# Performance work log

Hardware: AMD Instinct MI355X
Metric: run time of the kernel (lower is better)

Reference implementation:

```python
import jax, jax.numpy as jnp
import numpy as np

DV = 512   # node feature size
DE = 256   # edge feature size
N = 128    # valid node num (human_nums + obj_nums)
B = 8
K = 3      # propagate_layers
C = 117    # hoi_classes


def gru_cell(x, h, w_ih, w_hh, b_ih, b_hh):
    # PyTorch nn.GRU single step, gate order (r, z, n)
    gi = w_ih @ x + b_ih
    gh = w_hh @ h + b_hh
    ir, iz, inn = jnp.split(gi, 3)
    hr, hz, hn = jnp.split(gh, 3)
    r = jax.nn.sigmoid(ir + hr)
    z = jax.nn.sigmoid(iz + hz)
    n = jnp.tanh(inn + r * hn)
    return (1.0 - z) * n + z * h


def _run_graph(h, e, w_link, b_link, w_msg, b_msg, w_ih, w_hh, b_ih, b_hh):
    # h: [dv, N], e: [de, N, N]
    wl_j = w_link[:DV]          # applied to Feature[:dv, i, :] = h (column index j)
    wl_i = w_link[DV:2 * DV]    # applied to Feature[dv:2dv, :, i] = h (row index i)
    wl_e = w_link[2 * DV:]
    adj = jnp.zeros((N, N), h.dtype)
    for _ in range(K):
        # link function on Feature built under torch.no_grad -> stop_gradient
        hs = jax.lax.stop_gradient(h)
        es = jax.lax.stop_gradient(e)
        logits = (wl_i @ hs)[:, None] + (wl_j @ hs)[None, :] \
                 + jnp.einsum('c,cij->ij', wl_e, es) + b_link
        adj = jax.nn.sigmoid(logits)  # [N, N]

        def node_step(carry, i):
            h, e = carry
            h_v = h[:, i]                      # [dv]
            e_row = e[:, i, :]                 # [de, N] (rows < i already updated this round)
            comb = jnp.concatenate(
                [jnp.broadcast_to(h_v[:, None], (DV, N)), h, e_row], axis=0)  # [2dv+de, N]
            m = jax.nn.relu(w_msg @ comb + b_msg[:, None])                    # [de, N]
            e = e.at[:, i, :].set(m)
            m_sum = (m * adj[i][None, :]).sum(axis=1)                         # [de]
            h_new = gru_cell(m_sum, h_v, w_ih, w_hh, b_ih, b_hh)
            h = h.at[:, i].set(h_new)
            return (h, e), None

        (h, e), _ = jax.lax.scan(node_step, (h, e), jnp.arange(N))
    return adj, h


def setup_inputs() -> dict:
    key = jax.random.key(0)
    ks = jax.random.split(key, 8)
    s = 0.02
    return {
        "edge_features": jax.random.normal(ks[0], (B, N, N, DE), jnp.float32),
        "node_features": jax.random.normal(ks[1], (B, N, DV), jnp.float32),
        "adj_mat": jnp.zeros((B, N, N), jnp.float32),
        "node_labels": jnp.zeros((B, N, C), jnp.float32),
        "human_nums": jnp.full((B,), 32, jnp.int32),
        "obj_nums": jnp.full((B,), 96, jnp.int32),
        "w_link": jax.random.normal(ks[2], (2 * DV + DE,), jnp.float32) * s,
        "b_link": jnp.zeros((), jnp.float32),
        "w_msg": jax.random.normal(ks[3], (DE, 2 * DV + DE), jnp.float32) * s,
        "b_msg": jnp.zeros((DE,), jnp.float32),
        "w_ih": jax.random.normal(ks[4], (3 * DV, DE), jnp.float32) * s,
        "w_hh": jax.random.normal(ks[5], (3 * DV, DV), jnp.float32) * s,
        "b_ih": jnp.zeros((3 * DV,), jnp.float32),
        "b_hh": jnp.zeros((3 * DV,), jnp.float32),
        "w_ro": jax.random.normal(ks[6], (C, DV), jnp.float32) * s,
        "b_ro": jnp.zeros((C,), jnp.float32),
    }


def reference(edge_features, node_features, adj_mat, node_labels, human_nums,
              obj_nums, w_link, b_link, w_msg, b_msg, w_ih, w_hh, b_ih, b_hh,
              w_ro, b_ro):
    e0 = jnp.transpose(edge_features, (0, 3, 1, 2))  # [B, de, N, N]
    h0 = jnp.transpose(node_features, (0, 2, 1))     # [B, dv, N]
    run = jax.vmap(_run_graph, in_axes=(0, 0) + (None,) * 8)
    pred_adj_mat, h = run(h0, e0, w_link, b_link, w_msg, b_msg,
                          w_ih, w_hh, b_ih, b_hh)
    # readout on the final (post-last-update) node states
    pred_node_labels = jnp.einsum('cd,bdn->bnc', w_ro, h) + b_ro
    return pred_adj_mat, pred_node_labels
```

## Files before the change

kernel.cpp:

```cpp
#include <hip/hip_runtime.h>
#include <math.h>


#define NB 8
#define NN 128
#define DVV 512
#define DEE 256
#define NCC 117
#define SB 16
#define PGOFF 196608

typedef __attribute__((ext_vector_type(8))) short short8;
typedef __attribute__((ext_vector_type(4))) float f32x4;

__device__ __forceinline__ float sigmf(float x) {
  x = fminf(fmaxf(x, -30.f), 30.f);
  return 1.0f / (1.0f + __expf(-x));
}
__device__ __forceinline__ float tanhf_fast(float x) {
  x = fminf(fmaxf(x, -15.f), 15.f);
  float e = __expf(2.0f * x);
  return (e - 1.0f) / (e + 1.0f);
}
__device__ __forceinline__ unsigned short f2bf(float f) {
  union { float f; unsigned u; } v; v.f = f;
  unsigned u = v.u + 0x7FFFu + ((v.u >> 16) & 1u);
  return (unsigned short)(u >> 16);
}

__global__ __launch_bounds__(256) void k_copy(const float* __restrict__ src, float* __restrict__ dst) {
  int i = blockIdx.x * 256 + threadIdx.x;
  ((float4*)dst)[i] = ((const float4*)src)[i];
}

__global__ __launch_bounds__(256) void k_cvtw(const float* __restrict__ w_msg,
                                              unsigned short* __restrict__ w3b) {
  int idx = blockIdx.x * 256 + threadIdx.x;
  int r = idx >> 8, c = idx & 255;
  w3b[idx] = f2bf(w_msg[(size_t)r * 1280 + 1024 + c]);
}

__global__ __launch_bounds__(128) void k_av(const float* __restrict__ h, const float* __restrict__ w_link,
                                            float* __restrict__ av) {
  int b = blockIdx.x >> 7, n = blockIdx.x & 127;
  int lane = threadIdx.x & 63, half = threadIdx.x >> 6;
  const float* hc = h + (size_t)((b << 7) + n) * DVV;
  const float* w = w_link + half * DVV;
  float acc = 0.f;
#pragma unroll
  for (int t = 0; t < 8; ++t) { int d = lane + (t << 6); acc += w[d] * hc[d]; }
#pragma unroll
  for (int off = 32; off; off >>= 1) acc += __shfl_down(acc, off);
  if (lane == 0) av[(b << 8) + half * NN + n] = acc;
}

template <int FIRST>
__global__ __launch_bounds__(256) void k_plogit_mfma(
    const float* src, const unsigned short* __restrict__ w3b,
    const float* __restrict__ w_link, const float* __restrict__ av,
    const float* __restrict__ b_link, float* e_buf, float* __restrict__ adj_out) {
  int b = blockIdx.x >> 7, i = blockIdx.x & 127;
  __shared__ unsigned short eL[128 * 264];
  int tid = threadIdx.x;

  if (FIRST) {
    const float* s0 = src + (size_t)(b * NN + i) * NN * DEE;
    int j = tid >> 6, c0 = (tid & 63) * 4;
#pragma unroll 4
    for (int it = 0; it < 32; ++it, j += 4) {
      float4 v = *(const float4*)&s0[(size_t)j * DEE + c0];
      unsigned long long pk = (unsigned long long)f2bf(v.x)
                            | ((unsigned long long)f2bf(v.y) << 16)
                            | ((unsigned long long)f2bf(v.z) << 32)
                            | ((unsigned long long)f2bf(v.w) << 48);
      *(unsigned long long*)&eL[j * 264 + c0] = pk;
    }
  } else {
    const float* s0 = src + (size_t)(b * NN + i) * DEE * NN;
    int j0 = (tid & 31) * 4, c0b = (tid >> 5) * 4;
#pragma unroll
    for (int it = 0; it < 8; ++it) {
      int c0 = c0b + 32 * it;
      float4 r0 = *(const float4*)&s0[(size_t)(c0 + 0) * NN + j0];
      float4 r1 = *(const float4*)&s0[(size_t)(c0 + 1) * NN + j0];
      float4 r2 = *(const float4*)&s0[(size_t)(c0 + 2) * NN + j0];
      float4 r3 = *(const float4*)&s0[(size_t)(c0 + 3) * NN + j0];
      unsigned long long p0 = (unsigned long long)f2bf(r0.x) | ((unsigned long long)f2bf(r1.x) << 16)
                            | ((unsigned long long)f2bf(r2.x) << 32) | ((unsigned long long)f2bf(r3.x) << 48);
      unsigned long long p1 = (unsigned long long)f2bf(r0.y) | ((unsigned long long)f2bf(r1.y) << 16)
                            | ((unsigned long long)f2bf(r2.y) << 32) | ((unsigned long long)f2bf(r3.y) << 48);
      unsigned long long p2 = (unsigned long long)f2bf(r0.z) | ((unsigned long long)f2bf(r1.z) << 16)
                            | ((unsigned long long)f2bf(r2.z) << 32) | ((unsigned long long)f2bf(r3.z) << 48);
      unsigned long long p3 = (unsigned long long)f2bf(r0.w) | ((unsigned long long)f2bf(r1.w) << 16)
                            | ((unsigned long long)f2bf(r2.w) << 32) | ((unsigned long long)f2bf(r3.w) << 48);
      *(unsigned long long*)&eL[(j0 + 0) * 264 + c0] = p0;
      *(unsigned long long*)&eL[(j0 + 1) * 264 + c0] = p1;
      *(unsigned long long*)&eL[(j0 + 2) * 264 + c0] = p2;
      *(unsigned long long*)&eL[(j0 + 3) * 264 + c0] = p3;
    }
  }
  __syncthreads();

  float accLE = 0.f;
  if (tid < NN) {
    const unsigned short* row = &eL[tid * 264];
    for (int c = 0; c < DEE; ++c) {
      union { unsigned u; float f; } cv; cv.u = ((unsigned)row[c]) << 16;
      accLE += w_link[1024 + c] * cv.f;
    }
  }

  const int w = tid >> 6, l = tid & 63;
  const int lm = l & 15, lg = l >> 4;
  f32x4 acc[4][8];
#pragma unroll
  for (int a = 0; a < 4; ++a)
#pragma unroll
    for (int jt = 0; jt < 8; ++jt) acc[a][jt] = (f32x4){0.f, 0.f, 0.f, 0.f};

#pragma unroll
  for (int kk = 0; kk < 8; ++kk) {
    short8 afr[4];
#pragma unroll
    for (int a = 0; a < 4; ++a)
      afr[a] = *(const short8*)&w3b[(size_t)(64 * w + 16 * a + lm) * 256 + 32 * kk + 8 * lg];
#pragma unroll
    for (int jt = 0; jt < 8; ++jt) {
      short8 bfr = *(const short8*)&eL[(16 * jt + lm) * 264 + 32 * kk + 8 * lg];
#pragma unroll
      for (int a = 0; a < 4; ++a)
        acc[a][jt] = __builtin_amdgcn_mfma_f32_16x16x32_bf16(afr[a], bfr, acc[a][jt], 0, 0, 0);
    }
  }

  float* Pout = e_buf + (size_t)(b * NN + i) * DEE * NN;
#pragma unroll
  for (int a = 0; a < 4; ++a) {
    int rbase = 64 * w + 16 * a + 4 * lg;
#pragma unroll
    for (int jt = 0; jt < 8; ++jt) {
      int j = 16 * jt + lm;
#pragma unroll
      for (int q = 0; q < 4; ++q)
        Pout[(size_t)(rbase + q) * NN + j] = acc[a][jt][q];
    }
  }
  if (tid < NN) {
    float x = av[(b << 8) + NN + i] + av[(b << 8) + tid] + accLE + b_link[0];
    adj_out[((size_t)b * NN + i) * NN + tid] = sigmf(x);
  }
}

__global__ __launch_bounds__(256) void k_wh3(const float* __restrict__ w_hh, const float* __restrict__ w_msg,
                                             const float* __restrict__ b_hh, const float* __restrict__ b_msg,
                                             const float* __restrict__ h, float* __restrict__ GHo,
                                             float* __restrict__ Uo, float* __restrict__ Go) {
  int bx = blockIdx.x, b = blockIdx.y;
  const float* W; const float* bias; float* out; int ldw, R, r0;
  if (bx < 96)       { W = w_hh;        ldw = 512;  R = 1536; bias = b_hh;   out = GHo; r0 = bx * 16; }
  else if (bx < 112) { W = w_msg;       ldw = 1280; R = 256;  bias = b_msg;  out = Uo;  r0 = (bx - 96) * 16; }
  else               { W = w_msg + 512; ldw = 1280; R = 256;  bias = nullptr; out = Go; r0 = (bx - 112) * 16; }
  __shared__ float hT[128][129];
  __shared__ float wT[16][129];
  __shared__ float outT[16][129];
  int tid = threadIdx.x;
  int n = tid & 127, rr = tid >> 7;
  float acc8[8] = {0, 0, 0, 0, 0, 0, 0, 0};
  for (int dc = 0; dc < DVV; dc += 128) {
    if (dc) __syncthreads();
    for (int l = tid * 4; l < 16384; l += 1024) {
      int nn = l >> 7, d = l & 127;
      float4 v = *(const float4*)&h[((size_t)(b << 7) + nn) * DVV + dc + d];
      hT[d + 0][nn] = v.x; hT[d + 1][nn] = v.y; hT[d + 2][nn] = v.z; hT[d + 3][nn] = v.w;
    }
    for (int l = tid; l < 2048; l += 256) {
      int r = l >> 7, d = l & 127;
      wT[r][d] = W[(size_t)(r0 + r) * ldw + dc + d];
    }
    __syncthreads();
    for (int d = 0; d < 128; ++d) {
      float hval = hT[d][n];
#pragma unroll
      for (int r8 = 0; r8 < 8; ++r8) acc8[r8] += wT[rr * 8 + r8][d] * hval;
    }
  }
#pragma unroll
  for (int r8 = 0; r8 < 8; ++r8) {
    int r = rr * 8 + r8;
    outT[r][n] = acc8[r8] + (bias ? bias[r0 + r] : 0.0f);
  }
  __syncthreads();
  int n2 = tid >> 1, q = tid & 1;
  size_t base = ((size_t)(b << 7) + n2) * R + r0 + q * 8;
  float4 o0; o0.x = outT[q * 8 + 0][n2]; o0.y = outT[q * 8 + 1][n2]; o0.z = outT[q * 8 + 2][n2]; o0.w = outT[q * 8 + 3][n2];
  float4 o1; o1.x = outT[q * 8 + 4][n2]; o1.y = outT[q * 8 + 5][n2]; o1.z = outT[q * 8 + 6][n2]; o1.w = outT[q * 8 + 7][n2];
  *(float4*)&out[base] = o0;
  *(float4*)&out[base + 4] = o1;
}

template <int WRITE_E>
__global__ __launch_bounds__(256) void k_scan8(
    float* eP, const float* __restrict__ adj, const float* __restrict__ GH,
    const float* __restrict__ U, const float* __restrict__ Gini, float* __restrict__ h,
    const float* __restrict__ w_ih, const float* __restrict__ b_ih,
    const float* __restrict__ w_msg, float* __restrict__ pg,
    unsigned* __restrict__ flags, int kround) {
  const int s = blockIdx.x, b = blockIdx.y, tid = threadIdx.x;
  __shared__ float wihL[16 * 1540];
  __shared__ __align__(16) float w2L[16 * 520];
  __shared__ __align__(16) float GL[16 * 132];
  __shared__ float hnL[DVV];
  __shared__ float msL[16];

  for (int l = tid; l < 1536 * 16; l += 256) {
    int r = l >> 4, c = l & 15;
    wihL[c * 1540 + r] = w_ih[(size_t)r * 256 + 16 * s + c];
  }
  for (int l = tid; l < 16 * 128; l += 256) {
    int c = l >> 7, d4 = (l & 127) * 4;
    *(float4*)&w2L[c * 520 + d4] = *(const float4*)&w_msg[(size_t)(16 * s + c) * 1280 + 512 + d4];
  }
  for (int l = tid; l < 2048; l += 256) {
    int c = l & 15, j = l >> 4;
    GL[c * 132 + j] = Gini[((size_t)b * NN + j) * DEE + 16 * s + c];
  }
  float bi0 = b_ih[tid], bi1 = b_ih[tid + 256];
  float bi2 = b_ih[512 + tid], bi3 = b_ih[768 + tid];
  float bi4 = b_ih[1024 + tid], bi5 = b_ih[1280 + tid];

  const int c_loc = tid >> 4, jg = tid & 15, j0 = jg << 3;

  float4 P0, P1, A0, A1; float uu;
  float hv0, hv1, ghr0, ghr1, ghz0, ghz1, ghn0, ghn1;
  {
    size_t rE = ((size_t)(b * NN + 0) * DEE + 16 * s + c_loc) * NN + j0;
    P0 = *(const float4*)&eP[rE]; P1 = *(const float4*)&eP[rE + 4];
    size_t rA = (size_t)(b * NN + 0) * NN + j0;
    A0 = *(const float4*)&adj[rA]; A1 = *(const float4*)&adj[rA + 4];
    uu = U[(size_t)(b * NN + 0) * DEE + 16 * s + c_loc];
    size_t rH = (size_t)(b * NN + 0) * DVV;
    hv0 = h[rH + tid]; hv1 = h[rH + tid + 256];
    size_t rG = (size_t)(b * NN + 0) * 1536;
    ghr0 = GH[rG + tid]; ghr1 = GH[rG + tid + 256];
    ghz0 = GH[rG + 512 + tid]; ghz1 = GH[rG + 768 + tid];
    ghn0 = GH[rG + 1024 + tid]; ghn1 = GH[rG + 1280 + tid];
  }

  for (int i = 0; i < NN; ++i) {
    float* pgb = pg + (size_t)(i & 1) * PGOFF + (size_t)((b << 4) + s) * 1536;
    float* pgr = pg + (size_t)(i & 1) * PGOFF + (size_t)(b << 4) * 1536;
    __syncthreads();

    float acc;
    {
      const float* gl = &GL[c_loc * 132 + j0];
      float4 g0 = *(const float4*)&gl[0];
      float4 g1 = *(const float4*)&gl[4];
      float m0 = fmaxf(uu + g0.x + P0.x, 0.f), m1 = fmaxf(uu + g0.y + P0.y, 0.f);
      float m2 = fmaxf(uu + g0.z + P0.z, 0.f), m3 = fmaxf(uu + g0.w + P0.w, 0.f);
      float m4 = fmaxf(uu + g1.x + P1.x, 0.f), m5 = fmaxf(uu + g1.y + P1.y, 0.f);
      float m6 = fmaxf(uu + g1.z + P1.z, 0.f), m7 = fmaxf(uu + g1.w + P1.w, 0.f);
      acc = A0.x * m0 + A0.y * m1 + A0.z * m2 + A0.w * m3
          + A1.x * m4 + A1.y * m5 + A1.z * m6 + A1.w * m7;
      if (WRITE_E) {
        size_t rE = ((size_t)(b * NN + i) * DEE + 16 * s + c_loc) * NN + j0;
        float4 w0; w0.x = m0; w0.y = m1; w0.z = m2; w0.w = m3;
        float4 w1; w1.x = m4; w1.y = m5; w1.z = m6; w1.w = m7;
        *(float4*)&eP[rE] = w0; *(float4*)&eP[rE + 4] = w1;
      }
    }
    {
      int in = (i < NN - 1) ? i + 1 : NN - 1;
      size_t rE = ((size_t)(b * NN + in) * DEE + 16 * s + c_loc) * NN + j0;
      P0 = *(const float4*)&eP[rE]; P1 = *(const float4*)&eP[rE + 4];
      size_t rA = (size_t)(b * NN + in) * NN + j0;
      A0 = *(const float4*)&adj[rA]; A1 = *(const float4*)&adj[rA + 4];
      uu = U[(size_t)(b * NN + in) * DEE + 16 * s + c_loc];
    }
    acc += __shfl_down(acc, 8);
    acc += __shfl_down(acc, 4);
    acc += __shfl_down(acc, 2);
    acc += __shfl_down(acc, 1);
    if (jg == 0) msL[c_loc] = acc;
    __syncthreads();

    {
      float ms[16];
#pragma unroll
      for (int c = 0; c < 16; ++c) ms[c] = msL[c];
#pragma unroll
      for (int u = 0; u < 6; ++u) {
        int r = tid + (u << 8);
        float pa = 0.f;
#pragma unroll
        for (int c = 0; c < 16; ++c) pa += wihL[c * 1540 + r] * ms[c];
        __hip_atomic_store(&pgb[r], pa, __ATOMIC_RELAXED, __HIP_MEMORY_SCOPE_SYSTEM);
      }
    }

    {
      unsigned tgt = (unsigned)(kround * NN + i + 1);
      __syncthreads();
      if (tid < 64) {
        if (tid == 0)
          __hip_atomic_store(&flags[(((b << 4) + s) << 5)], tgt, __ATOMIC_RELAXED,
                             __HIP_MEMORY_SCOPE_SYSTEM);
        unsigned* fp = &flags[(((b << 4) + (tid & 15)) << 5)];
        for (;;) {
          unsigned v = __hip_atomic_load(fp, __ATOMIC_RELAXED, __HIP_MEMORY_SCOPE_SYSTEM);
          if (!__any(v < tgt)) break;
          __builtin_amdgcn_s_sleep(1);
        }
      }
      __syncthreads();
    }

    {
      float sr0 = bi0, sr1 = bi1, sz0 = bi2, sz1 = bi3, sn0 = bi4, sn1 = bi5;
#pragma unroll
      for (int ss = 0; ss < 16; ++ss) {
        float* p = pgr + (size_t)ss * 1536;
        sr0 += __hip_atomic_load(&p[tid],        __ATOMIC_RELAXED, __HIP_MEMORY_SCOPE_SYSTEM);
        sr1 += __hip_atomic_load(&p[tid + 256],  __ATOMIC_RELAXED, __HIP_MEMORY_SCOPE_SYSTEM);
        sz0 += __hip_atomic_load(&p[512 + tid],  __ATOMIC_RELAXED, __HIP_MEMORY_SCOPE_SYSTEM);
        sz1 += __hip_atomic_load(&p[768 + tid],  __ATOMIC_RELAXED, __HIP_MEMORY_SCOPE_SYSTEM);
        sn0 += __hip_atomic_load(&p[1024 + tid], __ATOMIC_RELAXED, __HIP_MEMORY_SCOPE_SYSTEM);
        sn1 += __hip_atomic_load(&p[1280 + tid], __ATOMIC_RELAXED, __HIP_MEMORY_SCOPE_SYSTEM);
      }
      float rg0 = sigmf(sr0 + ghr0), rg1 = sigmf(sr1 + ghr1);
      float z0 = sigmf(sz0 + ghz0),  z1 = sigmf(sz1 + ghz1);
      float nv0 = tanhf_fast(sn0 + rg0 * ghn0);
      float nv1 = tanhf_fast(sn1 + rg1 * ghn1);
      float hn0 = (1.f - z0) * nv0 + z0 * hv0;
      float hn1 = (1.f - z1) * nv1 + z1 * hv1;
      hnL[tid] = hn0; hnL[tid + 256] = hn1;
      size_t rH = (size_t)(b * NN + i) * DVV;
      if ((tid >> 5) == s) h[rH + tid] = hn0;
      if (((tid + 256) >> 5) == s) h[rH + tid + 256] = hn1;
    }
    {
      int in = (i < NN - 1) ? i + 1 : NN - 1;
      size_t rH = (size_t)(b * NN + in) * DVV;
      hv0 = h[rH + tid]; hv1 = h[rH + tid + 256];
      size_t rG = (size_t)(b * NN + in) * 1536;
      ghr0 = GH[rG + tid]; ghr1 = GH[rG + tid + 256];
      ghz0 = GH[rG + 512 + tid]; ghz1 = GH[rG + 768 + tid];
      ghn0 = GH[rG + 1024 + tid]; ghn1 = GH[rG + 1280 + tid];
    }
    __syncthreads();

    {
      int cw = tid >> 4, dg = tid & 15;
      float acc2 = 0.f;
#pragma unroll
      for (int it = 0; it < 32; ++it) {
        int d = dg + (it << 4);
        acc2 += w2L[cw * 520 + d] * hnL[d];
      }
      acc2 += __shfl_down(acc2, 8);
      acc2 += __shfl_down(acc2, 4);
      acc2 += __shfl_down(acc2, 2);
      acc2 += __shfl_down(acc2, 1);
      if (dg == 0) GL[cw * 132 + i] = acc2;
    }
  }
}

__global__ __launch_bounds__(128) void k_labels(const float* __restrict__ h, const float* __restrict__ w_ro,
                                                const float* __restrict__ b_ro, float* __restrict__ out) {
  int b = blockIdx.x >> 7, n = blockIdx.x & 127;
  __shared__ __align__(16) float hr[512];
  int tid = threadIdx.x;
  *(float4*)&hr[tid * 4] = *(const float4*)&h[(size_t)((b << 7) + n) * DVV + tid * 4];
  __syncthreads();
  if (tid < NCC) {
    const float* w = w_ro + (size_t)tid * DVV;
    float acc = b_ro[tid];
    for (int d = 0; d < DVV; d += 4) {
      float4 wv = *(const float4*)&w[d];
      acc += wv.x * hr[d] + wv.y * hr[d + 1] + wv.z * hr[d + 2] + wv.w * hr[d + 3];
    }
    out[(size_t)((b << 7) + n) * NCC + tid] = acc;
  }
}

extern "C" void kernel_launch(void* const* d_in, const int* in_sizes, int n_in,
                              void* d_out, int out_size, void* d_ws, size_t ws_size,
                              hipStream_t stream) {
  const float* edge   = (const float*)d_in[0];
  const float* node   = (const float*)d_in[1];
  const float* w_link = (const float*)d_in[6];
  const float* b_link = (const float*)d_in[7];
  const float* w_msg  = (const float*)d_in[8];
  const float* b_msg  = (const float*)d_in[9];
  const float* w_ih   = (const float*)d_in[10];
  const float* w_hh   = (const float*)d_in[11];
  const float* b_ih   = (const float*)d_in[12];
  const float* b_hh   = (const float*)d_in[13];
  const float* w_ro   = (const float*)d_in[14];
  const float* b_ro   = (const float*)d_in[15];
  float* out = (float*)d_out;
  float* ws  = (float*)d_ws;

  float* e_buf  = ws;
  float* h_buf  = e_buf + 33554432ull;
  float* GH_buf = h_buf + 524288;
  float* U_buf  = GH_buf + 1572864;
  float* G_buf  = U_buf + 262144;
  float* lE_buf = G_buf + 262144;
  float* av_buf = lE_buf + 131072;
  float* pg_buf = av_buf + 2048;
  unsigned* flags = (unsigned*)(pg_buf + 2 * PGOFF);
  unsigned short* w3b = (unsigned short*)lE_buf;
  size_t need_bytes = 36710304ull * 4ull;
  if (ws_size < need_bytes) return;

  hipMemsetAsync(flags, 0, 4096 * sizeof(unsigned), stream);
  k_copy<<<512, 256, 0, stream>>>(node, h_buf);
  k_cvtw<<<256, 256, 0, stream>>>(w_msg, w3b);

  for (int k = 0; k < 3; ++k) {
    k_av<<<1024, 128, 0, stream>>>(h_buf, w_link, av_buf);
    if (k == 0) k_plogit_mfma<1><<<1024, 256, 0, stream>>>(edge, w3b, w_link, av_buf, b_link, e_buf, out);
    else        k_plogit_mfma<0><<<1024, 256, 0, stream>>>(e_buf, w3b, w_link, av_buf, b_link, e_buf, out);
    k_wh3<<<dim3(128, 8), 256, 0, stream>>>(w_hh, w_msg, b_hh, b_msg, h_buf, GH_buf, U_buf, G_buf);
    if (k < 2) k_scan8<1><<<dim3(SB, NB), 256, 0, stream>>>(e_buf, out, GH_buf, U_buf, G_buf, h_buf,
                                                            w_ih, b_ih, w_msg, pg_buf, flags, k);
    else       k_scan8<0><<<dim3(SB, NB), 256, 0, stream>>>(e_buf, out, GH_buf, U_buf, G_buf, h_buf,
                                                            w_ih, b_ih, w_msg, pg_buf, flags, k);
  }
  k_labels<<<1024, 128, 0, stream>>>(h_buf, w_ro, b_ro, out + 131072);
}
```

Before: 2.313 ms.

## Store edge workspace in bf16 to halve edge buffer traffic

The large per-edge projection/message buffer moves from fp32 to bf16 storage. The plogit kernel writes bf16 and reads it back with a short8 transpose into LDS, and the scan kernel loads and stores short8 instead of two float4s. A bf16 copy of h is also kept, though nothing reads it yet. This cuts memory traffic on the dominant edge buffer, at the cost of extra rounding error in the stored messages that compounds across the three rounds.

New measurement: 2.310 ms. About the same (-0.1%).

```diff
diff --git a/kernel.cpp b/kernel.cpp
--- a/kernel.cpp
+++ b/kernel.cpp
@@ -27,10 +27,18 @@
   unsigned u = v.u + 0x7FFFu + ((v.u >> 16) & 1u);
   return (unsigned short)(u >> 16);
 }
-
-__global__ __launch_bounds__(256) void k_copy(const float* __restrict__ src, float* __restrict__ dst) {
+__device__ __forceinline__ float bfu(unsigned short u) {
+  union { unsigned u; float f; } v; v.u = ((unsigned)u) << 16; return v.f;
+}
+
+__global__ __launch_bounds__(256) void k_copy(const float* __restrict__ src, float* __restrict__ dst,
+                                              unsigned short* __restrict__ hb) {
   int i = blockIdx.x * 256 + threadIdx.x;
-  ((float4*)dst)[i] = ((const float4*)src)[i];
+  float4 v = ((const float4*)src)[i];
+  ((float4*)dst)[i] = v;
+  unsigned long long pk = (unsigned long long)f2bf(v.x) | ((unsigned long long)f2bf(v.y) << 16)
+                        | ((unsigned long long)f2bf(v.z) << 32) | ((unsigned long long)f2bf(v.w) << 48);
+  *(unsigned long long*)&hb[i * 4] = pk;
 }
 
 __global__ __launch_bounds__(256) void k_cvtw(const float* __restrict__ w_msg,
@@ -56,47 +64,43 @@
 
 template <int FIRST>
 __global__ __launch_bounds__(256) void k_plogit_mfma(
-    const float* src, const unsigned short* __restrict__ w3b,
+    const float* edge, const unsigned short* eP16in, const unsigned short* __restrict__ w3b,
     const float* __restrict__ w_link, const float* __restrict__ av,
-    const float* __restrict__ b_link, float* e_buf, float* __restrict__ adj_out) {
+    const float* __restrict__ b_link, unsigned short* eP16out, float* __restrict__ adj_out) {
   int b = blockIdx.x >> 7, i = blockIdx.x & 127;
   __shared__ unsigned short eL[128 * 264];
   int tid = threadIdx.x;
 
   if (FIRST) {
-    const float* s0 = src + (size_t)(b * NN + i) * NN * DEE;
-    int j = tid >> 6, c0 = (tid & 63) * 4;
-#pragma unroll 4
-    for (int it = 0; it < 32; ++it, j += 4) {
-      float4 v = *(const float4*)&s0[(size_t)j * DEE + c0];
-      unsigned long long pk = (unsigned long long)f2bf(v.x)
-                            | ((unsigned long long)f2bf(v.y) << 16)
-                            | ((unsigned long long)f2bf(v.z) << 32)
-                            | ((unsigned long long)f2bf(v.w) << 48);
-      *(unsigned long long*)&eL[j * 264 + c0] = pk;
+    const float* s0 = edge + (size_t)(b * NN + i) * NN * DEE;
+    for (int l = tid; l < 4096; l += 256) {
+      int j = l >> 5, c0 = (l & 31) * 8;
+      float4 v0 = *(const float4*)&s0[(size_t)j * DEE + c0];
+      float4 v1 = *(const float4*)&s0[(size_t)j * DEE + c0 + 4];
+      unsigned long long p0 = (unsigned long long)f2bf(v0.x) | ((unsigned long long)f2bf(v0.y) << 16)
+                            | ((unsigned long long)f2bf(v0.z) << 32) | ((unsigned long long)f2bf(v0.w) << 48);
+      unsigned long long p1 = (unsigned long long)f2bf(v1.x) | ((unsigned long long)f2bf(v1.y) << 16)
+                            | ((unsigned long long)f2bf(v1.z) << 32) | ((unsigned long long)f2bf(v1.w) << 48);
+      *(unsigned long long*)&eL[j * 264 + c0] = p0;
+      *(unsigned long long*)&eL[j * 264 + c0 + 4] = p1;
     }
   } else {
-    const float* s0 = src + (size_t)(b * NN + i) * DEE * NN;
-    int j0 = (tid & 31) * 4, c0b = (tid >> 5) * 4;
-#pragma unroll
-    for (int it = 0; it < 8; ++it) {
-      int c0 = c0b + 32 * it;
-      float4 r0 = *(const float4*)&s0[(size_t)(c0 + 0) * NN + j0];
-      float4 r1 = *(const float4*)&s0[(size_t)(c0 + 1) * NN + j0];
-      float4 r2 = *(const float4*)&s0[(size_t)(c0 + 2) * NN + j0];
-      float4 r3 = *(const float4*)&s0[(size_t)(c0 + 3) * NN + j0];
-      unsigned long long p0 = (unsigned long long)f2bf(r0.x) | ((unsigned long long)f2bf(r1.x) << 16)
-                            | ((unsigned long long)f2bf(r2.x) << 32) | ((unsigned long long)f2bf(r3.x) << 48);
-      unsigned long long p1 = (unsigned long long)f2bf(r0.y) | ((unsigned long long)f2bf(r1.y) << 16)
-                            | ((unsigned long long)f2bf(r2.y) << 32) | ((unsigned long long)f2bf(r3.y) << 48);
-      unsigned long long p2 = (unsigned long long)f2bf(r0.z) | ((unsigned long long)f2bf(r1.z) << 16)
-                            | ((unsigned long long)f2bf(r2.z) << 32) | ((unsigned long long)f2bf(r3.z) << 48);
-      unsigned long long p3 = (unsigned long long)f2bf(r0.w) | ((unsigned long long)f2bf(r1.w) << 16)
-                            | ((unsigned long long)f2bf(r2.w) << 32) | ((unsigned long long)f2bf(r3.w) << 48);
-      *(unsigned long long*)&eL[(j0 + 0) * 264 + c0] = p0;
-      *(unsigned long long*)&eL[(j0 + 1) * 264 + c0] = p1;
-      *(unsigned long long*)&eL[(j0 + 2) * 264 + c0] = p2;
-      *(unsigned long long*)&eL[(j0 + 3) * 264 + c0] = p3;
+    const unsigned short* s0 = eP16in + (size_t)(b * NN + i) * DEE * NN;
+#pragma unroll
+    for (int t = 0; t < 2; ++t) {
+      int blk = tid + t * 256;
+      int c0 = (blk >> 4) * 8, j0 = (blk & 15) * 8;
+      short8 rows[8];
+#pragma unroll
+      for (int cc = 0; cc < 8; ++cc)
+        rows[cc] = *(const short8*)&s0[(size_t)(c0 + cc) * NN + j0];
+#pragma unroll
+      for (int jj = 0; jj < 8; ++jj) {
+        short8 o;
+#pragma unroll
+        for (int cc = 0; cc < 8; ++cc) o[cc] = rows[cc][jj];
+        *(short8*)&eL[(j0 + jj) * 264 + c0] = o;
+      }
     }
   }
   __syncthreads();
@@ -104,10 +108,7 @@
   float accLE = 0.f;
   if (tid < NN) {
     const unsigned short* row = &eL[tid * 264];
-    for (int c = 0; c < DEE; ++c) {
-      union { unsigned u; float f; } cv; cv.u = ((unsigned)row[c]) << 16;
-      accLE += w_link[1024 + c] * cv.f;
-    }
+    for (int c = 0; c < DEE; ++c) accLE += w_link[1024 + c] * bfu(row[c]);
   }
 
   const int w = tid >> 6, l = tid & 63;
@@ -133,7 +134,7 @@
     }
   }
 
-  float* Pout = e_buf + (size_t)(b * NN + i) * DEE * NN;
+  unsigned short* Pout = eP16out + (size_t)(b * NN + i) * DEE * NN;
 #pragma unroll
   for (int a = 0; a < 4; ++a) {
     int rbase = 64 * w + 16 * a + 4 * lg;
@@ -142,7 +143,7 @@
       int j = 16 * jt + lm;
 #pragma unroll
       for (int q = 0; q < 4; ++q)
-        Pout[(size_t)(rbase + q) * NN + j] = acc[a][jt][q];
+        Pout[(size_t)(rbase + q) * NN + j] = f2bf(acc[a][jt][q]);
     }
   }
   if (tid < NN) {
@@ -199,12 +200,12 @@
 }
 
 template <int WRITE_E>
-__global__ __launch_bounds__(256) void k_scan8(
-    float* eP, const float* __restrict__ adj, const float* __restrict__ GH,
+__global__ __launch_bounds__(256) void k_scan10(
+    unsigned short* eP16, const float* __restrict__ adj, const float* __restrict__ GH,
     const float* __restrict__ U, const float* __restrict__ Gini, float* __restrict__ h,
-    const float* __restrict__ w_ih, const float* __restrict__ b_ih,
-    const float* __restrict__ w_msg, float* __restrict__ pg,
-    unsigned* __restrict__ flags, int kround) {
+    unsigned short* __restrict__ hb, const float* __restrict__ w_ih,
+    const float* __restrict__ b_ih, const float* __restrict__ w_msg,
+    float* __restrict__ pg, unsigned* __restrict__ flags, int kround) {
   const int s = blockIdx.x, b = blockIdx.y, tid = threadIdx.x;
   __shared__ float wihL[16 * 1540];
   __shared__ __align__(16) float w2L[16 * 520];
@@ -230,11 +231,11 @@
 
   const int c_loc = tid >> 4, jg = tid & 15, j0 = jg << 3;
 
-  float4 P0, P1, A0, A1; float uu;
+  short8 Pv; float4 A0, A1; float uu;
   float hv0, hv1, ghr0, ghr1, ghz0, ghz1, ghn0, ghn1;
   {
     size_t rE = ((size_t)(b * NN + 0) * DEE + 16 * s + c_loc) * NN + j0;
-    P0 = *(const float4*)&eP[rE]; P1 = *(const float4*)&eP[rE + 4];
+    Pv = *(const short8*)&eP16[rE];
     size_t rA = (size_t)(b * NN + 0) * NN + j0;
     A0 = *(const float4*)&adj[rA]; A1 = *(const float4*)&adj[rA + 4];
     uu = U[(size_t)(b * NN + 0) * DEE + 16 * s + c_loc];
@@ -256,23 +257,28 @@
       const float* gl = &GL[c_loc * 132 + j0];
       float4 g0 = *(const float4*)&gl[0];
       float4 g1 = *(const float4*)&gl[4];
-      float m0 = fmaxf(uu + g0.x + P0.x, 0.f), m1 = fmaxf(uu + g0.y + P0.y, 0.f);
-      float m2 = fmaxf(uu + g0.z + P0.z, 0.f), m3 = fmaxf(uu + g0.w + P0.w, 0.f);
-      float m4 = fmaxf(uu + g1.x + P1.x, 0.f), m5 = fmaxf(uu + g1.y + P1.y, 0.f);
-      float m6 = fmaxf(uu + g1.z + P1.z, 0.f), m7 = fmaxf(uu + g1.w + P1.w, 0.f);
+      float m0 = fmaxf(uu + g0.x + bfu((unsigned short)Pv[0]), 0.f);
+      float m1 = fmaxf(uu + g0.y + bfu((unsigned short)Pv[1]), 0.f);
+      float m2 = fmaxf(uu + g0.z + bfu((unsigned short)Pv[2]), 0.f);
+      float m3 = fmaxf(uu + g0.w + bfu((unsigned short)Pv[3]), 0.f);
+      float m4 = fmaxf(uu + g1.x + bfu((unsigned short)Pv[4]), 0.f);
+      float m5 = fmaxf(uu + g1.y + bfu((unsigned short)Pv[5]), 0.f);
+      float m6 = fmaxf(uu + g1.z + bfu((unsigned short)Pv[6]), 0.f);
+      float m7 = fmaxf(uu + g1.w + bfu((unsigned short)Pv[7]), 0.f);
       acc = A0.x * m0 + A0.y * m1 + A0.z * m2 + A0.w * m3
           + A1.x * m4 + A1.y * m5 + A1.z * m6 + A1.w * m7;
       if (WRITE_E) {
         size_t rE = ((size_t)(b * NN + i) * DEE + 16 * s + c_loc) * NN + j0;
-        float4 w0; w0.x = m0; w0.y = m1; w0.z = m2; w0.w = m3;
-        float4 w1; w1.x = m4; w1.y = m5; w1.z = m6; w1.w = m7;
-        *(float4*)&eP[rE] = w0; *(float4*)&eP[rE + 4] = w1;
+        short8 mw;
+        mw[0] = (short)f2bf(m0); mw[1] = (short)f2bf(m1); mw[2] = (short)f2bf(m2); mw[3] = (short)f2bf(m3);
+        mw[4] = (short)f2bf(m4); mw[5] = (short)f2bf(m5); mw[6] = (short)f2bf(m6); mw[7] = (short)f2bf(m7);
+        *(short8*)&eP16[rE] = mw;
       }
     }
     {
       int in = (i < NN - 1) ? i + 1 : NN - 1;
       size_t rE = ((size_t)(b * NN + in) * DEE + 16 * s + c_loc) * NN + j0;
-      P0 = *(const float4*)&eP[rE]; P1 = *(const float4*)&eP[rE + 4];
+      Pv = *(const short8*)&eP16[rE];
       size_t rA = (size_t)(b * NN + in) * NN + j0;
       A0 = *(const float4*)&adj[rA]; A1 = *(const float4*)&adj[rA + 4];
       uu = U[(size_t)(b * NN + in) * DEE + 16 * s + c_loc];
@@ -335,8 +341,8 @@
       float hn1 = (1.f - z1) * nv1 + z1 * hv1;
       hnL[tid] = hn0; hnL[tid + 256] = hn1;
       size_t rH = (size_t)(b * NN + i) * DVV;
-      if ((tid >> 5) == s) h[rH + tid] = hn0;
-      if (((tid + 256) >> 5) == s) h[rH + tid + 256] = hn1;
+      if ((tid >> 5) == s)         { h[rH + tid] = hn0;       hb[rH + tid] = f2bf(hn0); }
+      if (((tid + 256) >> 5) == s) { h[rH + tid + 256] = hn1; hb[rH + tid + 256] = f2bf(hn1); }
     }
     {
       int in = (i < NN - 1) ? i + 1 : NN - 1;
@@ -402,8 +408,9 @@
   float* out = (float*)d_out;
   float* ws  = (float*)d_ws;
 
-  float* e_buf  = ws;
-  float* h_buf  = e_buf + 33554432ull;
+  unsigned short* eP16 = (unsigned short*)ws;
+  unsigned short* hb   = (unsigned short*)(ws + 21000000);
+  float* h_buf  = ws + 33554432ull;
   float* GH_buf = h_buf + 524288;
   float* U_buf  = GH_buf + 1572864;
   float* G_buf  = U_buf + 262144;
@@ -416,18 +423,18 @@
   if (ws_size < need_bytes) return;
 
   hipMemsetAsync(flags, 0, 4096 * sizeof(unsigned), stream);
-  k_copy<<<512, 256, 0, stream>>>(node, h_buf);
+  k_copy<<<512, 256, 0, stream>>>(node, h_buf, hb);
   k_cvtw<<<256, 256, 0, stream>>>(w_msg, w3b);
 
   for (int k = 0; k < 3; ++k) {
     k_av<<<1024, 128, 0, stream>>>(h_buf, w_link, av_buf);
-    if (k == 0) k_plogit_mfma<1><<<1024, 256, 0, stream>>>(edge, w3b, w_link, av_buf, b_link, e_buf, out);
-    else        k_plogit_mfma<0><<<1024, 256, 0, stream>>>(e_buf, w3b, w_link, av_buf, b_link, e_buf, out);
+    if (k == 0) k_plogit_mfma<1><<<1024, 256, 0, stream>>>(edge, eP16, w3b, w_link, av_buf, b_link, eP16, out);
+    else        k_plogit_mfma<0><<<1024, 256, 0, stream>>>(edge, eP16, w3b, w_link, av_buf, b_link, eP16, out);
     k_wh3<<<dim3(128, 8), 256, 0, stream>>>(w_hh, w_msg, b_hh, b_msg, h_buf, GH_buf, U_buf, G_buf);
-    if (k < 2) k_scan8<1><<<dim3(SB, NB), 256, 0, stream>>>(e_buf, out, GH_buf, U_buf, G_buf, h_buf,
-                                                            w_ih, b_ih, w_msg, pg_buf, flags, k);
-    else       k_scan8<0><<<dim3(SB, NB), 256, 0, stream>>>(e_buf, out, GH_buf, U_buf, G_buf, h_buf,
-                                                            w_ih, b_ih, w_msg, pg_buf, flags, k);
+    if (k < 2) k_scan10<1><<<dim3(SB, NB), 256, 0, stream>>>(eP16, out, GH_buf, U_buf, G_buf, h_buf, hb,
+                                                             w_ih, b_ih, w_msg, pg_buf, flags, k);
+    else       k_scan10<0><<<dim3(SB, NB), 256, 0, stream>>>(eP16, out, GH_buf, U_buf, G_buf, h_buf, hb,
+                                                             w_ih, b_ih, w_msg, pg_buf, flags, k);
   }
   k_labels<<<1024, 128, 0, stream>>>(h_buf, w_ro, b_ro, out + 131072);
 }
```
